# Kernel tuning notes

Measured on AMD Instinct MI355X. Metric: run time of the kernel, lower is better.

The kernel has to match this reference:

```python
import jax, jax.numpy as jnp
import numpy as np

N, M, K, R, D = 2048, 64, 2, 512, 1024   # seq len, chunk size, neighbours, neighbour len, model dim
H, L = 16, 1024                           # heads, layer_size
LCH = N // M                              # number of chunks l = 32
DH = L // H
SCALE = 1.0 / (D ** 0.5)                  # source scales by input dim, not head dim


def setup_inputs() -> dict:
    key = jax.random.key(0)
    ks = jax.random.split(key, 6)
    s = 0.02
    return {
        "x": jax.random.normal(ks[0], (N, D), jnp.float32),
        "neighbours": jax.random.normal(ks[1], (LCH, K, R, D), jnp.float32),
        "Wq": jax.random.normal(ks[2], (L, D), jnp.float32) * s,
        "Wk": jax.random.normal(ks[3], (L, D), jnp.float32) * s,
        "Wv": jax.random.normal(ks[4], (L, D), jnp.float32) * s,
        "Wo": jax.random.normal(ks[5], (D, L), jnp.float32) * s,
    }


def _attend(q_in, ctx, Wq, Wk, Wv, Wo):
    # q_in: (B, Q, D) queries; ctx: (B, K, R, D) retrieved neighbours.
    # Batches the per-chunk, per-neighbour Attention calls of the source in one pass,
    # then means over the K neighbour axis (reduce 'k m d -> m d', 'mean').
    B, Q = q_in.shape[0], q_in.shape[1]
    q = (q_in @ Wq.T).reshape(B, Q, H, DH)                     # (B,Q,H,DH)
    kk = (ctx @ Wk.T).reshape(B, K, R, H, DH)                  # (B,K,R,H,DH)
    vv = (ctx @ Wv.T).reshape(B, K, R, H, DH)
    scores = jnp.einsum('bqhe,bkrhe->bkhrq', q, kk) * SCALE    # (B,K,H,R,Q)
    # FAITHFUL quirk: source softmaxes over the QUERY axis (last dim of 'b k q')
    w = jax.nn.softmax(scores, axis=-1)
    o = jnp.einsum('bkhrq,bkrhe->bkqhe', w, vv).reshape(B, K, Q, L)
    z = jnp.einsum('bkql,dl->bkqd', o, Wo)                     # output projection (dropout=0)
    return z.mean(axis=1)                                      # mean over neighbours -> (B,Q,D)


def reference(x, neighbours, Wq, Wk, Wv, Wo):
    # attending_chunks: shift input left by m-1, zero-pad bottom, chunk into (l, m, d)
    att = jnp.concatenate([x[M - 1:], jnp.zeros((M - 1, D), x.dtype)], axis=0).reshape(LCH, M, D)
    # main loop over chunks u in [0, l-2] and their k neighbours, fully batched
    main = _attend(att[:LCH - 1], neighbours[:LCH - 1], Wq, Wk, Wv, Wo)   # (l-1, M, D)
    # last token attends to neighbours[-1]
    last = _attend(x[-1][None, None, :], neighbours[-1][None], Wq, Wk, Wv, Wo)  # (1,1,D)
    body = jnp.concatenate([main.reshape(-1, D), att[-1]], axis=0)        # (N, D)
    # pad top with m-1 zeros, keep first n rows
    out = jnp.concatenate([jnp.zeros((M - 1, D), x.dtype), body[:N - M + 1]], axis=0)
    out = out.at[:M - 1].set(x[:M - 1])
    out = out.at[-1].set(last[0, 0])
    return out
```

## Files before the change

kernel.cpp:

```cpp
#include <hip/hip_runtime.h>
#include <hip/hip_bf16.h>


using u16 = unsigned short;
using u32 = unsigned int;

typedef float  f32x4   __attribute__((ext_vector_type(4)));
typedef __bf16 bf16x8v __attribute__((ext_vector_type(8)));
typedef __bf16 bf16x4v __attribute__((ext_vector_type(4)));
typedef short  s16x4   __attribute__((ext_vector_type(4)));
typedef u16    u16x8   __attribute__((ext_vector_type(8)));
typedef u16    u16x4v  __attribute__((ext_vector_type(4)));

#define SCALE_LOG2E (1.4426950408889634f / 32.0f)

__device__ __forceinline__ u16 f2b(float f){ return __builtin_bit_cast(u16, (__bf16)f); }
__device__ __forceinline__ int swz(int row, int cb){ return row*128 + (cb ^ ((row & 7) << 4)); }

__device__ __forceinline__ void gl_lds16(const void* g, void* l) {
    __builtin_amdgcn_global_load_lds(
        (const __attribute__((address_space(1))) unsigned int*)(unsigned long long)g,
        (__attribute__((address_space(3))) unsigned int*)(unsigned int)(unsigned long long)l,
        16, 0, 0);
}

template<int OM>
__global__ __launch_bounds__(512, 2)
void gemm256(const u16* __restrict__ Ap, int lda,
             const u16* __restrict__ Bp, int ldb,
             void* __restrict__ Cp, void* __restrict__ Cp2,
             int M, int Kc, int nNt)
{
    __shared__ char Ls[131072];
    char* const Abase = Ls;
    char* const Bbase = Ls + 65536;

    const int tid  = threadIdx.x;
    const int lane = tid & 63, wave = tid >> 6;
    const int li = lane & 15, lg = lane >> 4;
    const int wr = wave >> 2, wc = wave & 3;

    const int nwg  = gridDim.x;
    const int lin  = blockIdx.x;
    const int lin2 = (lin & 7) * (nwg >> 3) + (lin >> 3);
    const long bm = (long)(lin2 / nNt) * 256;
    const long bn = (long)(lin2 % nNt) * 256;

    const int srow = tid >> 3;
    const int scol = ((tid & 7) ^ (srow & 7)) << 3;

    auto stageA = [&](int t, int hh) {
        char* d = Abase + (t & 1)*32768 + hh*16384 + wave*1024;
        long r0 = bm + hh*128 + srow;      if (r0 >= M) r0 = M - 1;
        long r1 = bm + hh*128 + 64 + srow; if (r1 >= M) r1 = M - 1;
        gl_lds16(Ap + r0*(long)lda + (long)t*64 + scol, d);
        gl_lds16(Ap + r1*(long)lda + (long)t*64 + scol, d + 8192);
    };
    auto stageB = [&](int t, int hh) {
        char* d = Bbase + (t & 1)*32768 + hh*16384 + wave*1024;
        long r0 = bn + hh*128 + srow;
        gl_lds16(Bp + r0*(long)ldb + (long)t*64 + scol, d);
        gl_lds16(Bp + (r0 + 64)*(long)ldb + (long)t*64 + scol, d + 8192);
    };

    const int NT = Kc >> 6;

    stageB(0, 0); stageB(0, 1); stageA(0, 0); stageA(0, 1); stageB(1, 0);
    asm volatile("s_waitcnt vmcnt(2)" ::: "memory");
    asm volatile("s_barrier" ::: "memory");

    const int swx = (li & 7) << 4;
    const int cb0 = (lg*16) ^ swx;
    const int cb1 = (64 + lg*16) ^ swx;
    const int arb = li;
    const int brb = (wc & 1)*64 + li;

    f32x4 acc[8][4] = {};
    bf16x8v a[4], b[4];

#define MFMA16(MH)                                                              \
    __builtin_amdgcn_s_setprio(1);                                              \
    _Pragma("unroll") for (int mt = 0; mt < 4; mt++)                            \
        _Pragma("unroll") for (int nt = 0; nt < 4; nt++)                        \
            acc[(MH)*4 + mt][nt] = __builtin_amdgcn_mfma_f32_16x16x32_bf16(     \
                a[mt], b[nt], acc[(MH)*4 + mt][nt], 0, 0, 0);                   \
    __builtin_amdgcn_s_setprio(0);

#define BAR_IN()  asm volatile("s_barrier" ::: "memory");                       \
                  asm volatile("s_waitcnt lgkmcnt(0)" ::: "memory");            \
                  __builtin_amdgcn_sched_barrier(0);
#define BAR_OUT() asm volatile("s_barrier" ::: "memory");

    for (int t = 0; t < NT - 1; ++t) {
        char* At = Abase + (t & 1)*32768 + wr*16384;
        char* Bt = Bbase + (t & 1)*32768 + (wc >> 1)*16384;

        #pragma unroll
        for (int mt = 0; mt < 4; mt++) a[mt] = *(const bf16x8v*)(At + (arb + mt*16)*128 + cb0);
        #pragma unroll
        for (int nt = 0; nt < 4; nt++) b[nt] = *(const bf16x8v*)(Bt + (brb + nt*16)*128 + cb0);
        stageB(t + 1, 1);
        BAR_IN(); MFMA16(0); BAR_OUT();
        #pragma unroll
        for (int mt = 0; mt < 4; mt++) a[mt] = *(const bf16x8v*)(At + (arb + 64 + mt*16)*128 + cb0);
        stageA(t + 1, 0);
        BAR_IN(); MFMA16(1); BAR_OUT();
        #pragma unroll
        for (int mt = 0; mt < 4; mt++) a[mt] = *(const bf16x8v*)(At + (arb + mt*16)*128 + cb1);
        #pragma unroll
        for (int nt = 0; nt < 4; nt++) b[nt] = *(const bf16x8v*)(Bt + (brb + nt*16)*128 + cb1);
        stageA(t + 1, 1);
        BAR_IN(); MFMA16(0); BAR_OUT();
        #pragma unroll
        for (int mt = 0; mt < 4; mt++) a[mt] = *(const bf16x8v*)(At + (arb + 64 + mt*16)*128 + cb1);
        if (t + 2 < NT) stageB(t + 2, 0);
        BAR_IN(); MFMA16(1);
        asm volatile("s_waitcnt vmcnt(2)" ::: "memory");
        BAR_OUT();
    }
    {
        const int t = NT - 1;
        char* At = Abase + (t & 1)*32768 + wr*16384;
        char* Bt = Bbase + (t & 1)*32768 + (wc >> 1)*16384;
        asm volatile("s_waitcnt vmcnt(0)" ::: "memory");
        asm volatile("s_barrier" ::: "memory");
        #pragma unroll
        for (int mt = 0; mt < 4; mt++) a[mt] = *(const bf16x8v*)(At + (arb + mt*16)*128 + cb0);
        #pragma unroll
        for (int nt = 0; nt < 4; nt++) b[nt] = *(const bf16x8v*)(Bt + (brb + nt*16)*128 + cb0);
        BAR_IN(); MFMA16(0); BAR_OUT();
        #pragma unroll
        for (int mt = 0; mt < 4; mt++) a[mt] = *(const bf16x8v*)(At + (arb + 64 + mt*16)*128 + cb0);
        BAR_IN(); MFMA16(1); BAR_OUT();
        #pragma unroll
        for (int mt = 0; mt < 4; mt++) a[mt] = *(const bf16x8v*)(At + (arb + mt*16)*128 + cb1);
        #pragma unroll
        for (int nt = 0; nt < 4; nt++) b[nt] = *(const bf16x8v*)(Bt + (brb + nt*16)*128 + cb1);
        BAR_IN(); MFMA16(0); BAR_OUT();
        #pragma unroll
        for (int mt = 0; mt < 4; mt++) a[mt] = *(const bf16x8v*)(At + (arb + 64 + mt*16)*128 + cb1);
        BAR_IN(); MFMA16(1); BAR_OUT();
    }
#undef MFMA16
#undef BAR_IN
#undef BAR_OUT

    if (OM == 3 && bn >= 1024) {
        u16* Vt = (u16*)Cp2;
        #pragma unroll
        for (int ai = 0; ai < 8; ai++) {
            const int m0 = wr*128 + (ai >> 2)*64 + (ai & 3)*16 + lg*4;
            #pragma unroll
            for (int nt = 0; nt < 4; nt++) {
                const int n = wc*64 + nt*16 + li;
                f32x4 c = acc[ai][nt];
                bf16x4v w;
                #pragma unroll
                for (int j = 0; j < 4; j++) w[j] = (__bf16)c[j];
                *(bf16x4v*)(Ls + n*512 + ((m0*2) ^ ((n & 31) << 4))) = w;
            }
        }
        __syncthreads();
        const int n    = tid >> 1;
        const int half = (tid & 1) * 128;
        u16* dst = Vt + (bn - 1024 + n)*32768L + bm + half;
        #pragma unroll
        for (int i = 0; i < 16; i++) {
            const int mb = (half + i*8) * 2;
            uint4 v = *(const uint4*)(Ls + n*512 + (mb ^ ((n & 31) << 4)));
            *(uint4*)(dst + i*8) = v;
        }
    } else if (OM == 3) {
        u16* Ka = (u16*)Cp;
        #pragma unroll
        for (int ai = 0; ai < 8; ai++) {
            #pragma unroll
            for (int nt = 0; nt < 4; nt++) {
                f32x4 c = acc[ai][nt];
                const long row0 = bm + wr*128 + (ai >> 2)*64 + (ai & 3)*16 + lg*4;
                const long col  = bn + wc*64 + nt*16 + li;
                #pragma unroll
                for (int j = 0; j < 4; j++) {
                    long rg = row0 + j;
                    if (rg < M) Ka[rg*1024 + col] = f2b(c[j]);
                }
            }
        }
    }
}

template<bool AF32, int OM>
__global__ __launch_bounds__(256)
void gemm128(const void* __restrict__ Ap, int lda,
             const u16* __restrict__ Bp, int ldb,
             void* __restrict__ Cp, void* __restrict__ Cp2,
             int M, int Kc, int row_off, int nNt)
{
    __shared__ char As[128*128];
    __shared__ char Bs[128*128];
    const int tid  = threadIdx.x;
    const int lane = tid & 63, wave = tid >> 6;
    const int li = lane & 15, lg = lane >> 4;
    const int wr = wave >> 1, wc = wave & 1;

    const int nwg  = gridDim.x;
    const int lin  = blockIdx.x;
    const int lin2 = (lin & 7) * (nwg >> 3) + (lin >> 3);
    const long bm = (long)(lin2 / nNt) * 128;
    const long bn = (long)(lin2 % nNt) * 128;

    const int grow = wave*32 + (lane >> 3);
    const int gcol = ((lane & 7) ^ (lane >> 3)) << 3;
    const int sr = tid >> 1, sc = (tid & 1) * 32;
    long arow_f = bm + sr; if (arow_f >= M) arow_f = M - 1;
    long arow_g[4];
    #pragma unroll
    for (int j = 0; j < 4; j++) {
        long r = bm + grow + j*8;
        arow_g[j] = (r < M) ? r : (M - 1);
    }

    f32x4 acc[4][4] = {};

    for (int k0 = 0; k0 < Kc; k0 += 64) {
        float4 a4[8];
        if (AF32) {
            const float4* ap = (const float4*)((const float*)Ap + arow_f*lda + k0 + sc);
            #pragma unroll
            for (int i = 0; i < 8; i++) a4[i] = ap[i];
        }
        __syncthreads();
        if (!AF32) {
            #pragma unroll
            for (int j = 0; j < 4; j++)
                gl_lds16((const u16*)Ap + arow_g[j]*(long)lda + k0 + gcol,
                         As + (wave*4 + j)*1024);
        }
        #pragma unroll
        for (int j = 0; j < 4; j++)
            gl_lds16(Bp + (bn + grow + j*8)*(long)ldb + k0 + gcol,
                     Bs + (wave*4 + j)*1024);
        if (AF32) {
            #pragma unroll
            for (int i = 0; i < 4; i++) {
                float4 f0 = a4[2*i], f1 = a4[2*i+1];
                bf16x8v w;
                w[0]=(__bf16)f0.x; w[1]=(__bf16)f0.y; w[2]=(__bf16)f0.z; w[3]=(__bf16)f0.w;
                w[4]=(__bf16)f1.x; w[5]=(__bf16)f1.y; w[6]=(__bf16)f1.z; w[7]=(__bf16)f1.w;
                *(bf16x8v*)(As + swz(sr, sc*2 + i*16)) = w;
            }
        }
        __syncthreads();
        #pragma unroll
        for (int es = 0; es < 2; es++) {
            bf16x8v af[4], bfv[4];
            #pragma unroll
            for (int mt = 0; mt < 4; mt++)
                af[mt] = *(const bf16x8v*)(As + swz(wr*64 + mt*16 + li, es*64 + lg*16));
            #pragma unroll
            for (int nt = 0; nt < 4; nt++)
                bfv[nt] = *(const bf16x8v*)(Bs + swz(wc*64 + nt*16 + li, es*64 + lg*16));
            #pragma unroll
            for (int mt = 0; mt < 4; mt++)
                #pragma unroll
                for (int nt = 0; nt < 4; nt++)
                    acc[mt][nt] = __builtin_amdgcn_mfma_f32_16x16x32_bf16(
                        af[mt], bfv[nt], acc[mt][nt], 0, 0, 0);
        }
    }

    #pragma unroll
    for (int mt = 0; mt < 4; mt++) {
        #pragma unroll
        for (int nt = 0; nt < 4; nt++) {
            f32x4 c = acc[mt][nt];
            const long row0 = bm + wr*64 + mt*16 + lg*4;
            const long col  = bn + wc*64 + nt*16 + li;
            if (OM == 0) {
                u16* C = (u16*)Cp;
                #pragma unroll
                for (int j = 0; j < 4; j++) {
                    long rg = row0 + j;
                    if (rg < M) C[rg*1024 + col] = f2b(c[j]);
                }
            } else if (OM == 2) {
                float* C = (float*)Cp;
                #pragma unroll
                for (int j = 0; j < 4; j++) {
                    long rg = row0 + j;
                    if (rg < M) C[(row_off + rg)*1024 + col] = c[j];
                }
            } else {
                if (col < 1024) {
                    u16* Ka = (u16*)Cp;
                    #pragma unroll
                    for (int j = 0; j < 4; j++) Ka[(row0 + j)*1024 + col] = f2b(c[j]);
                } else {
                    u16* Vt = (u16*)Cp2;
                    bf16x4v w;
                    #pragma unroll
                    for (int j = 0; j < 4; j++) w[j] = (__bf16)c[j];
                    *(bf16x4v*)(Vt + (col - 1024)*32768L + row0) = w;
                }
            }
        }
    }
}

__global__ __launch_bounds__(256)
void attn_kernel(const u16* __restrict__ Qa, const u16* __restrict__ Ka,
                 const u16* __restrict__ Vt, u16* __restrict__ Om)
{
    const int u = blockIdx.x, h = blockIdx.y;
    const int tid = threadIdx.x;
    const int lane = tid & 63, wave = tid >> 6;
    const int li = lane & 15, lg = lane >> 4;

    bf16x8v qf[4][2];
    #pragma unroll
    for (int qt = 0; qt < 4; qt++)
        #pragma unroll
        for (int es = 0; es < 2; es++)
            qf[qt][es] = *(const bf16x8v*)(Qa + (long)(63 + u*64 + qt*16 + li)*1024
                                              + h*64 + es*32 + lg*8);

    f32x4 acc[4][4] = {};

    for (int it = wave; it < 64; it += 4) {
        const int k = it >> 5, rsub = it & 31;
        const long kr = (long)u*1024 + k*512 + rsub*16;

        bf16x8v a0 = *(const bf16x8v*)(Ka + (kr + li)*1024 + h*64 + lg*8);
        bf16x8v a1 = *(const bf16x8v*)(Ka + (kr + li)*1024 + h*64 + 32 + lg*8);
        f32x4 s[4];
        #pragma unroll
        for (int qt = 0; qt < 4; qt++) {
            f32x4 c = {};
            c = __builtin_amdgcn_mfma_f32_16x16x32_bf16(a0, qf[qt][0], c, 0, 0, 0);
            c = __builtin_amdgcn_mfma_f32_16x16x32_bf16(a1, qf[qt][1], c, 0, 0, 0);
            s[qt] = c;
        }
        float p[4][4];
        #pragma unroll
        for (int qt = 0; qt < 4; qt++)
            #pragma unroll
            for (int j = 0; j < 4; j++)
                p[qt][j] = __builtin_amdgcn_exp2f(s[qt][j]);
        float rz[4];
        #pragma unroll
        for (int j = 0; j < 4; j++) {
            float z = p[0][j] + p[1][j] + p[2][j] + p[3][j];
            z += __shfl_xor(z, 1); z += __shfl_xor(z, 2);
            z += __shfl_xor(z, 4); z += __shfl_xor(z, 8);
            rz[j] = __builtin_amdgcn_rcpf(z);
        }
        s16x4 wf[4];
        #pragma unroll
        for (int qt = 0; qt < 4; qt++) {
            bf16x4v w;
            #pragma unroll
            for (int j = 0; j < 4; j++) w[j] = (__bf16)(p[qt][j] * rz[j]);
            wf[qt] = __builtin_bit_cast(s16x4, w);
        }
        #pragma unroll
        for (int et = 0; et < 4; et++) {
            s16x4 va = *(const s16x4*)(Vt + (long)(h*64 + et*16 + li)*32768 + kr + lg*4);
            #pragma unroll
            for (int qt = 0; qt < 4; qt++)
                acc[et][qt] = __builtin_amdgcn_mfma_f32_16x16x16bf16_1k(
                    va, wf[qt], acc[et][qt], 0, 0, 0);
        }
    }

    __shared__ float Osum[64*64];
    for (int w = 0; w < 4; w++) {
        if (wave == w) {
            #pragma unroll
            for (int et = 0; et < 4; et++)
                #pragma unroll
                for (int qt = 0; qt < 4; qt++)
                    #pragma unroll
                    for (int j = 0; j < 4; j++) {
                        int e = et*16 + lg*4 + j, q = qt*16 + li;
                        if (w == 0) Osum[e*64 + q]  = acc[et][qt][j];
                        else        Osum[e*64 + q] += acc[et][qt][j];
                    }
        }
        __syncthreads();
    }
    const int q = tid & 63, e0 = (tid >> 6) * 16;
    u16x8 o0, o1;
    #pragma unroll
    for (int i = 0; i < 8; i++) {
        o0[i] = f2b(0.5f * Osum[(e0 + i    )*64 + q]);
        o1[i] = f2b(0.5f * Osum[(e0 + 8 + i)*64 + q]);
    }
    u16* dst = Om + (long)(u*64 + q)*1024 + h*64 + e0;
    *(u16x8*)dst       = o0;
    *(u16x8*)(dst + 8) = o1;
}

__global__ __launch_bounds__(256)
void convert_w(const float* __restrict__ Wq, const float* __restrict__ Wk,
               const float* __restrict__ Wv, const float* __restrict__ Wo,
               u16* __restrict__ dst)
{
    int idx = blockIdx.x*256 + threadIdx.x;
    int w   = idx >> 18;
    int off = (idx & 262143) << 2;
    const float* src = (w == 0) ? Wq : (w == 1) ? Wk : (w == 2) ? Wv : Wo;
    float scv = (w == 0) ? SCALE_LOG2E : 1.0f;
    float4 v = *(const float4*)(src + off);
    u16x4v o = { f2b(v.x*scv), f2b(v.y*scv), f2b(v.z*scv), f2b(v.w*scv) };
    *(u16x4v*)(dst + (long)w*1048576 + off) = o;
}

__global__ __launch_bounds__(256)
void convert_a(const float* __restrict__ src, u16* __restrict__ dst, int n8)
{
    int i = blockIdx.x*256 + threadIdx.x;
    const int stride = gridDim.x*256;
    for (; i < n8; i += stride) {
        float4 f0 = ((const float4*)src)[2*i], f1 = ((const float4*)src)[2*i+1];
        u16x8 o = { f2b(f0.x), f2b(f0.y), f2b(f0.z), f2b(f0.w),
                    f2b(f1.x), f2b(f1.y), f2b(f1.z), f2b(f1.w) };
        ((u16x8*)dst)[i] = o;
    }
}

__global__ __launch_bounds__(256)
void last_kernel(const u16* __restrict__ Vt, u16* __restrict__ Om)
{
    const int row  = blockIdx.x*4 + (threadIdx.x >> 6);
    const int lane = threadIdx.x & 63;
    const u16* p = Vt + (long)row*32768 + 31*1024 + lane*16;
    float s = 0.f;
    #pragma unroll
    for (int hf = 0; hf < 2; hf++) {
        bf16x8v v = *(const bf16x8v*)(p + hf*8);
        #pragma unroll
        for (int i = 0; i < 8; i++) s += (float)v[i];
    }
    #pragma unroll
    for (int m = 1; m < 64; m <<= 1) s += __shfl_xor(s, m);
    if (lane == 0) Om[(long)1984*1024 + row] = f2b(0.5f * s);
}

__global__ __launch_bounds__(256)
void copy_head(const float* __restrict__ x, float* __restrict__ out)
{
    int i = blockIdx.x*256 + threadIdx.x;
    ((float4*)out)[i] = ((const float4*)x)[i];
}

extern "C" void kernel_launch(void* const* d_in, const int* in_sizes, int n_in,
                              void* d_out, int out_size, void* d_ws, size_t ws_size,
                              hipStream_t stream)
{
    const float* x  = (const float*)d_in[0];
    const float* nb = (const float*)d_in[1];
    const float* Wq = (const float*)d_in[2];
    const float* Wk = (const float*)d_in[3];
    const float* Wv = (const float*)d_in[4];
    const float* Wo = (const float*)d_in[5];
    float* out = (float*)d_out;
    char*  ws  = (char*)d_ws;

    if (ws_size < (size_t)144*1024*1024) return;
    const bool big = ws_size >= (size_t)212*1024*1024;
    u16* wW  = (u16*)ws;
    u16* Qa  = (u16*)(ws + (size_t) 8*1024*1024);
    u16* Om  = (u16*)(ws + (size_t)12*1024*1024);
    u16* Ka  = (u16*)(ws + (size_t)16*1024*1024);
    u16* Vt  = (u16*)(ws + (size_t)80*1024*1024);
    u16* Anb = (u16*)(ws + (size_t)144*1024*1024);
    u16* xb  = (u16*)(ws + (size_t)208*1024*1024);
    u16* wWq = wW, *wWk = wW + 1048576, *wWo = wW + 3*1048576;

    convert_w<<<dim3(4096), dim3(256), 0, stream>>>(Wq, Wk, Wv, Wo, wW);

    if (big) {
        convert_a<<<dim3(2048), dim3(256), 0, stream>>>(nb, Anb, 4194304);
        convert_a<<<dim3(512),  dim3(256), 0, stream>>>(x,  xb,  262144);
        gemm128<false, 0><<<dim3(128), dim3(256), 0, stream>>>(
            xb, 1024, wWq, 1024, Qa, nullptr, 2048, 1024, 0, 8);
        gemm256<3><<<dim3(1024), dim3(512), 0, stream>>>(
            Anb, 1024, wWk, 1024, Ka, Vt, 32768, 1024, 8);
    } else {
        gemm128<true, 0><<<dim3(128), dim3(256), 0, stream>>>(
            x, 1024, wWq, 1024, Qa, nullptr, 2048, 1024, 0, 8);
        gemm128<true, 3><<<dim3(4096), dim3(256), 0, stream>>>(
            nb, 1024, wWk, 1024, Ka, Vt, 32768, 1024, 0, 16);
    }

    attn_kernel<<<dim3(31, 16), dim3(256), 0, stream>>>(Qa, Ka, Vt, Om);
    last_kernel<<<dim3(256),    dim3(256), 0, stream>>>(Vt, Om);

    gemm128<false, 2><<<dim3(128), dim3(256), 0, stream>>>(
        Om, 1024, wWo, 1024, out, nullptr, 1985, 1024, 63, 8);
    copy_head<<<dim3(63), dim3(256), 0, stream>>>(x, out);
}
```

Measured before the change: 262.4 us.

## Simplify GEMM main loop to two 32-MFMA phases with whole-tile prefetch

Restructures the GEMM K-loop from four 16-MFMA phases with staggered half-tile global->LDS prefetches into two 32-MFMA phases. All A/B fragments for a k-half are read at once and the whole next tile is issued at the start of each iteration. This halves the barrier count per tile and removes the peeled last iteration. The cost is more VGPRs (8 A fragments live) and a coarser prefetch schedule that waits with vmcnt(0) each iteration, so less global-load latency may be hidden.

```diff
diff --git a/kernel.cpp b/kernel.cpp
--- a/kernel.cpp
+++ b/kernel.cpp
@@ -65,8 +65,8 @@
 
     const int NT = Kc >> 6;
 
-    stageB(0, 0); stageB(0, 1); stageA(0, 0); stageA(0, 1); stageB(1, 0);
-    asm volatile("s_waitcnt vmcnt(2)" ::: "memory");
+    stageA(0, 0); stageA(0, 1); stageB(0, 0); stageB(0, 1);
+    asm volatile("s_waitcnt vmcnt(0)" ::: "memory");
     asm volatile("s_barrier" ::: "memory");
 
     const int swx = (li & 7) << 4;
@@ -76,74 +76,48 @@
     const int brb = (wc & 1)*64 + li;
 
     f32x4 acc[8][4] = {};
-    bf16x8v a[4], b[4];
-
-#define MFMA16(MH)                                                              \
+    bf16x8v a[8], b[4];
+
+#define MFMA32()                                                                \
     __builtin_amdgcn_s_setprio(1);                                              \
-    _Pragma("unroll") for (int mt = 0; mt < 4; mt++)                            \
-        _Pragma("unroll") for (int nt = 0; nt < 4; nt++)                        \
-            acc[(MH)*4 + mt][nt] = __builtin_amdgcn_mfma_f32_16x16x32_bf16(     \
-                a[mt], b[nt], acc[(MH)*4 + mt][nt], 0, 0, 0);                   \
+    _Pragma("unroll") for (int mh = 0; mh < 2; mh++)                            \
+        _Pragma("unroll") for (int mt = 0; mt < 4; mt++)                        \
+            _Pragma("unroll") for (int nt = 0; nt < 4; nt++)                    \
+                acc[mh*4 + mt][nt] = __builtin_amdgcn_mfma_f32_16x16x32_bf16(   \
+                    a[mh*4 + mt], b[nt], acc[mh*4 + mt][nt], 0, 0, 0);          \
     __builtin_amdgcn_s_setprio(0);
 
 #define BAR_IN()  asm volatile("s_barrier" ::: "memory");                       \
                   asm volatile("s_waitcnt lgkmcnt(0)" ::: "memory");            \
                   __builtin_amdgcn_sched_barrier(0);
 #define BAR_OUT() asm volatile("s_barrier" ::: "memory");
-
-    for (int t = 0; t < NT - 1; ++t) {
+#define RD_AB(CB)                                                               \
+    _Pragma("unroll") for (int mt = 0; mt < 4; mt++) {                          \
+        a[mt]     = *(const bf16x8v*)(At + (arb + mt*16)*128 + (CB));           \
+        a[4 + mt] = *(const bf16x8v*)(At + (arb + 64 + mt*16)*128 + (CB));      \
+    }                                                                           \
+    _Pragma("unroll") for (int nt = 0; nt < 4; nt++)                            \
+        b[nt] = *(const bf16x8v*)(Bt + (brb + nt*16)*128 + (CB));
+
+    for (int t = 0; t < NT; ++t) {
         char* At = Abase + (t & 1)*32768 + wr*16384;
         char* Bt = Bbase + (t & 1)*32768 + (wc >> 1)*16384;
 
-        #pragma unroll
-        for (int mt = 0; mt < 4; mt++) a[mt] = *(const bf16x8v*)(At + (arb + mt*16)*128 + cb0);
-        #pragma unroll
-        for (int nt = 0; nt < 4; nt++) b[nt] = *(const bf16x8v*)(Bt + (brb + nt*16)*128 + cb0);
-        stageB(t + 1, 1);
-        BAR_IN(); MFMA16(0); BAR_OUT();
-        #pragma unroll
-        for (int mt = 0; mt < 4; mt++) a[mt] = *(const bf16x8v*)(At + (arb + 64 + mt*16)*128 + cb0);
-        stageA(t + 1, 0);
-        BAR_IN(); MFMA16(1); BAR_OUT();
-        #pragma unroll
-        for (int mt = 0; mt < 4; mt++) a[mt] = *(const bf16x8v*)(At + (arb + mt*16)*128 + cb1);
-        #pragma unroll
-        for (int nt = 0; nt < 4; nt++) b[nt] = *(const bf16x8v*)(Bt + (brb + nt*16)*128 + cb1);
-        stageA(t + 1, 1);
-        BAR_IN(); MFMA16(0); BAR_OUT();
-        #pragma unroll
-        for (int mt = 0; mt < 4; mt++) a[mt] = *(const bf16x8v*)(At + (arb + 64 + mt*16)*128 + cb1);
-        if (t + 2 < NT) stageB(t + 2, 0);
-        BAR_IN(); MFMA16(1);
-        asm volatile("s_waitcnt vmcnt(2)" ::: "memory");
+        RD_AB(cb0);
+        if (t + 1 < NT) {
+            stageA(t + 1, 0); stageA(t + 1, 1);
+            stageB(t + 1, 0); stageB(t + 1, 1);
+        }
+        BAR_IN(); MFMA32(); BAR_OUT();
+        RD_AB(cb1);
+        BAR_IN(); MFMA32();
+        asm volatile("s_waitcnt vmcnt(0)" ::: "memory");
         BAR_OUT();
     }
-    {
-        const int t = NT - 1;
-        char* At = Abase + (t & 1)*32768 + wr*16384;
-        char* Bt = Bbase + (t & 1)*32768 + (wc >> 1)*16384;
-        asm volatile("s_waitcnt vmcnt(0)" ::: "memory");
-        asm volatile("s_barrier" ::: "memory");
-        #pragma unroll
-        for (int mt = 0; mt < 4; mt++) a[mt] = *(const bf16x8v*)(At + (arb + mt*16)*128 + cb0);
-        #pragma unroll
-        for (int nt = 0; nt < 4; nt++) b[nt] = *(const bf16x8v*)(Bt + (brb + nt*16)*128 + cb0);
-        BAR_IN(); MFMA16(0); BAR_OUT();
-        #pragma unroll
-        for (int mt = 0; mt < 4; mt++) a[mt] = *(const bf16x8v*)(At + (arb + 64 + mt*16)*128 + cb0);
-        BAR_IN(); MFMA16(1); BAR_OUT();
-        #pragma unroll
-        for (int mt = 0; mt < 4; mt++) a[mt] = *(const bf16x8v*)(At + (arb + mt*16)*128 + cb1);
-        #pragma unroll
-        for (int nt = 0; nt < 4; nt++) b[nt] = *(const bf16x8v*)(Bt + (brb + nt*16)*128 + cb1);
-        BAR_IN(); MFMA16(0); BAR_OUT();
-        #pragma unroll
-        for (int mt = 0; mt < 4; mt++) a[mt] = *(const bf16x8v*)(At + (arb + 64 + mt*16)*128 + cb1);
-        BAR_IN(); MFMA16(1); BAR_OUT();
-    }
-#undef MFMA16
+#undef MFMA32
 #undef BAR_IN
 #undef BAR_OUT
+#undef RD_AB
 
     if (OM == 3 && bn >= 1024) {
         u16* Vt = (u16*)Cp2;
```

Result: slower. 272.9 us (+4.0%).
